# Optimization experiments

Measured on AMD Instinct MI355X. Metric: run time of the kernel, lower is better.

Reference implementation:

```python
import jax, jax.numpy as jnp
import numpy as np

B, D, L, H = 8192, 1024, 64, 256

def setup_inputs() -> dict:
    key = jax.random.key(0)
    k_x, k_w1, k_b1, k_w2, k_b2 = jax.random.split(key, 5)
    # Stacked per-label parameters (equivalent to L independent 2-layer MLPs)
    lim1 = 1.0 / np.sqrt(D)
    lim2 = 1.0 / np.sqrt(H)
    return {
        "x": jax.random.normal(k_x, (B, D), dtype=jnp.float32),
        "W1": jax.random.uniform(k_w1, (L, D, H), dtype=jnp.float32, minval=-lim1, maxval=lim1),
        "b1": jax.random.uniform(k_b1, (L, H), dtype=jnp.float32, minval=-lim1, maxval=lim1),
        "W2": jax.random.uniform(k_w2, (L, H), dtype=jnp.float32, minval=-lim2, maxval=lim2),
        "b2": jax.random.uniform(k_b2, (L,), dtype=jnp.float32, minval=-lim2, maxval=lim2),
    }

def reference(x, W1, b1, W2, b2):
    # h: [B, L, H] = relu(x @ W1_l + b1_l) for every label l, as one batched GEMM
    h = jax.nn.relu(jnp.einsum('bd,ldh->blh', x, W1) + b1[None, :, :])
    # out: [B, L] = h_l @ W2_l + b2_l  (second Linear has output dim 1, squeezed)
    out = jnp.einsum('blh,lh->bl', h, W2) + b2[None, :]
    return out
```

## Files before the change

kernel.cpp:

```cpp
#include <hip/hip_runtime.h>
#include <stdint.h>

#define B_SZ 8192
#define D_SZ 1024
#define L_SZ 64
#define H_SZ 256

#define BM 256
#define BN 256
#define BK 64
#define NT (D_SZ / BK)

typedef __attribute__((ext_vector_type(8))) __bf16 bf16x8;
typedef __attribute__((ext_vector_type(4))) float f32x4;

typedef __attribute__((address_space(1))) void as1_void;
typedef __attribute__((address_space(3))) void as3_void;

static __device__ __forceinline__ void gload_lds16(const void* g, void* l) {
    __builtin_amdgcn_global_load_lds((as1_void*)g, (as3_void*)l, 16, 0, 0);
}

static __device__ __forceinline__ unsigned short f2bf(float f) {
    uint32_t u = __builtin_bit_cast(uint32_t, f);
    u += 0x7fffu + ((u >> 16) & 1u);
    return (unsigned short)(u >> 16);
}

__global__ void cvt_x_kernel(const float* __restrict__ x, unsigned short* __restrict__ xb) {
    int i = blockIdx.x * blockDim.x + threadIdx.x;
    const float4 v = reinterpret_cast<const float4*>(x)[i];
    ushort4 o;
    o.x = f2bf(v.x); o.y = f2bf(v.y); o.z = f2bf(v.z); o.w = f2bf(v.w);
    reinterpret_cast<ushort4*>(xb)[i] = o;
}

__global__ void transpose_w1_kernel(const float* __restrict__ w1, unsigned short* __restrict__ w1t) {
    __shared__ float tile[64][65];
    int b = blockIdx.x;
    int l  = b >> 6;
    int dt = (b >> 2) & 15;
    int ht = b & 3;
    int tx = threadIdx.x & 63;
    int ty = threadIdx.x >> 6;
    const float* src = w1 + (size_t)l * (D_SZ * H_SZ);
    #pragma unroll
    for (int r = 0; r < 64; r += 4)
        tile[r + ty][tx] = src[(size_t)(dt * 64 + r + ty) * H_SZ + ht * 64 + tx];
    __syncthreads();
    unsigned short* dst = w1t + (size_t)l * (H_SZ * D_SZ);
    #pragma unroll
    for (int r = 0; r < 64; r += 4)
        dst[(size_t)(ht * 64 + r + ty) * D_SZ + dt * 64 + tx] = f2bf(tile[tx][r + ty]);
}


#define SBAR asm volatile("s_barrier" ::: "memory")
#define VMW(n) asm volatile("s_waitcnt vmcnt(" #n ")" ::: "memory")

#define DS_READ_A(c, quad) do { \
    _Pragma("unroll") for (int j = 0; j < 2; ++j) { \
        const int rowh = ((quad)*2 + j)*16 + rl; \
        _Pragma("unroll") for (int ks = 0; ks < 2; ++ks) { \
            const int slot = (ks*4 + g) ^ (rowh & 7); \
            af[ks][j] = *reinterpret_cast<const bf16x8*>( \
                reinterpret_cast<const char*>(&ldsAB[c][0][wr][0]) + rowh*128 + slot*16); \
        } } } while(0)

#define DS_READ_B(c) do { \
    _Pragma("unroll") for (int nf = 0; nf < 4; ++nf) { \
        const int rowb = wc*64 + nf*16 + rl; \
        const int bh = rowb >> 7; \
        const int rowh = rowb & 127; \
        _Pragma("unroll") for (int ks = 0; ks < 2; ++ks) { \
            const int slot = (ks*4 + g) ^ (rowh & 7); \
            bf[ks][nf] = *reinterpret_cast<const bf16x8*>( \
                reinterpret_cast<const char*>(&ldsAB[c][1][bh][0]) + rowh*128 + slot*16); \
        } } } while(0)

#define MFMA_QUAD(quad) do { \
    __builtin_amdgcn_s_setprio(1); \
    _Pragma("unroll") for (int ks = 0; ks < 2; ++ks) \
    _Pragma("unroll") for (int j = 0; j < 2; ++j) \
    _Pragma("unroll") for (int nf = 0; nf < 4; ++nf) \
        acc[(quad)*2 + j][nf] = __builtin_amdgcn_mfma_f32_16x16x32_bf16( \
            af[ks][j], bf[ks][nf], acc[(quad)*2 + j][nf], 0, 0, 0); \
    __builtin_amdgcn_s_setprio(0); } while(0)

#define STAGE_A(t, h) do { \
    gload_lds16(aSrc[h][0] + (size_t)(t)*BK, &ldsAB[(t)&1][0][h][(wid*64)*8]); \
    gload_lds16(aSrc[h][1] + (size_t)(t)*BK, &ldsAB[(t)&1][0][h][(512 + wid*64)*8]); } while(0)

#define STAGE_B(t, h) do { \
    gload_lds16(bSrc[h][0] + (size_t)(t)*BK, &ldsAB[(t)&1][1][h][(wid*64)*8]); \
    gload_lds16(bSrc[h][1] + (size_t)(t)*BK, &ldsAB[(t)&1][1][h][(512 + wid*64)*8]); } while(0)

__global__ __launch_bounds__(512, 2) void ffn_gemm_kernel(
    const unsigned short* __restrict__ xb,
    const unsigned short* __restrict__ w1t,
    const float* __restrict__ b1,
    const float* __restrict__ w2,
    const float* __restrict__ b2,
    float* __restrict__ out)
{
    __shared__ unsigned short ldsAB[2][2][2][128 * 64];

    const int bid = blockIdx.x;
    const int wg  = ((bid & 7) << 8) + (bid >> 3);
    const int l   = wg >> 5;
    const int m0  = (wg & 31) * BM;

    const int tid  = threadIdx.x;
    const int wid  = tid >> 6;
    const int lane = tid & 63;
    const int wr   = wid >> 2;
    const int wc   = wid & 3;
    const int g    = lane >> 4;
    const int rl   = lane & 15;

    const unsigned short* aSrc[2][2];
    const unsigned short* bSrc[2][2];
    #pragma unroll
    for (int h = 0; h < 2; ++h)
        #pragma unroll
        for (int c2 = 0; c2 < 2; ++c2) {
            const int q  = c2 * 512 + tid;
            const int r  = q >> 3;
            const int kg = (q & 7) ^ (r & 7);
            aSrc[h][c2] = xb  + (size_t)(m0 + h * 128 + r) * D_SZ + kg * 8;
            bSrc[h][c2] = w1t + ((size_t)l * H_SZ + h * 128 + r) * D_SZ + kg * 8;
        }

    f32x4 acc[8][4];
    #pragma unroll
    for (int m = 0; m < 8; ++m)
        #pragma unroll
        for (int n = 0; n < 4; ++n) {
            acc[m][n][0] = 0.f; acc[m][n][1] = 0.f;
            acc[m][n][2] = 0.f; acc[m][n][3] = 0.f;
        }

    bf16x8 af[2][2], bf[2][4];

    STAGE_B(0, 0); STAGE_B(0, 1);
    STAGE_A(0, 0); STAGE_A(0, 1);
    STAGE_B(1, 0); STAGE_B(1, 1);
    VMW(4);
    SBAR;

    #pragma unroll 1
    for (int i = 0; i < 7; ++i) {
        const int t1 = 2 * i + 1, t2 = 2 * i + 2, t3 = 2 * i + 3;
        DS_READ_B(0); DS_READ_A(0, 0); STAGE_A(t1, 0); SBAR; MFMA_QUAD(0); SBAR;
        DS_READ_A(0, 1); STAGE_A(t1, 1); SBAR; MFMA_QUAD(1); SBAR;
        DS_READ_A(0, 2); STAGE_B(t2, 0); SBAR; MFMA_QUAD(2); SBAR;
        DS_READ_A(0, 3); STAGE_B(t2, 1); SBAR; MFMA_QUAD(3); VMW(4); SBAR;
        DS_READ_B(1); DS_READ_A(1, 0); STAGE_A(t2, 0); SBAR; MFMA_QUAD(0); SBAR;
        DS_READ_A(1, 1); STAGE_A(t2, 1); SBAR; MFMA_QUAD(1); SBAR;
        DS_READ_A(1, 2); STAGE_B(t3, 0); SBAR; MFMA_QUAD(2); SBAR;
        DS_READ_A(1, 3); STAGE_B(t3, 1); SBAR; MFMA_QUAD(3); VMW(4); SBAR;
    }
    DS_READ_B(0); DS_READ_A(0, 0); STAGE_A(15, 0); SBAR; MFMA_QUAD(0); SBAR;
    DS_READ_A(0, 1); STAGE_A(15, 1); SBAR; MFMA_QUAD(1); SBAR;
    DS_READ_A(0, 2); SBAR; MFMA_QUAD(2); SBAR;
    DS_READ_A(0, 3); SBAR; MFMA_QUAD(3); VMW(0); SBAR;
    DS_READ_B(1); DS_READ_A(1, 0); SBAR; MFMA_QUAD(0); SBAR;
    DS_READ_A(1, 1); SBAR; MFMA_QUAD(1); SBAR;
    DS_READ_A(1, 2); SBAR; MFMA_QUAD(2); SBAR;
    DS_READ_A(1, 3); SBAR; MFMA_QUAD(3); SBAR;

    float b1v[4], w2v[4];
    #pragma unroll
    for (int nf = 0; nf < 4; ++nf) {
        const int col = wc * 64 + nf * 16 + rl;
        b1v[nf] = b1[l * H_SZ + col];
        w2v[nf] = w2[l * H_SZ + col];
    }
    __syncthreads();
    float* partLds = (float*)&ldsAB[0][0][0][0];
    #pragma unroll
    for (int mf = 0; mf < 8; ++mf) {
        #pragma unroll
        for (int r = 0; r < 4; ++r) {
            float p = 0.f;
            #pragma unroll
            for (int nf = 0; nf < 4; ++nf) {
                float v = acc[mf][nf][r] + b1v[nf];
                v = fmaxf(v, 0.f);
                p += v * w2v[nf];
            }
            p += __shfl_xor(p, 1);
            p += __shfl_xor(p, 2);
            p += __shfl_xor(p, 4);
            p += __shfl_xor(p, 8);
            if (rl == 0)
                partLds[((wr * 128) + mf * 16 + g * 4 + r) * 4 + wc] = p;
        }
    }
    __syncthreads();
    if (tid < BM) {
        float s = b2[l];
        #pragma unroll
        for (int w = 0; w < 4; ++w) s += partLds[tid * 4 + w];
        out[(size_t)(m0 + tid) * L_SZ + l] = s;
    }
}

extern "C" void kernel_launch(void* const* d_in, const int* in_sizes, int n_in,
                              void* d_out, int out_size, void* d_ws, size_t ws_size,
                              hipStream_t stream) {
    const float* x  = (const float*)d_in[0];
    const float* W1 = (const float*)d_in[1];
    const float* b1 = (const float*)d_in[2];
    const float* W2 = (const float*)d_in[3];
    const float* b2 = (const float*)d_in[4];
    float* out = (float*)d_out;

    unsigned short* xb  = (unsigned short*)d_ws;
    unsigned short* w1t = xb + (size_t)B_SZ * D_SZ;

    cvt_x_kernel<<<(B_SZ * D_SZ / 4) / 256, 256, 0, stream>>>(x, xb);
    transpose_w1_kernel<<<L_SZ * 16 * 4, 256, 0, stream>>>(W1, w1t);
    ffn_gemm_kernel<<<(B_SZ / BM) * L_SZ, 512, 0, stream>>>(xb, w1t, b1, W2, b2, out);
}
```

Baseline: 294.3 us.

## Make GEMM persistent over eight M-tiles, prefetching next tile during tail

The launch drops from 2048 workgroups to 256. Each workgroup now loops over eight consecutive 256-row M tiles for a fixed label and keeps bias/W2 values in registers. The last k-steps of one tile issue the loads for the next tile's first k-tiles, which hides the pipeline prologue and epilogue. The trade-off is only 256 workgroups on the GPU (about one per CU), so the occupancy of two blocks per CU is lost, plus a larger serial epilogue per workgroup. The final iteration prefetches past the tile range, into rows of the next group or past the end of xb.

```diff
diff --git a/kernel.cpp b/kernel.cpp
--- a/kernel.cpp
+++ b/kernel.cpp
@@ -9,7 +9,6 @@
 #define BM 256
 #define BN 256
 #define BK 64
-#define NT (D_SZ / BK)
 
 typedef __attribute__((ext_vector_type(8))) __bf16 bf16x8;
 typedef __attribute__((ext_vector_type(4))) float f32x4;
@@ -91,6 +90,10 @@
     gload_lds16(aSrc[h][0] + (size_t)(t)*BK, &ldsAB[(t)&1][0][h][(wid*64)*8]); \
     gload_lds16(aSrc[h][1] + (size_t)(t)*BK, &ldsAB[(t)&1][0][h][(512 + wid*64)*8]); } while(0)
 
+#define STAGE_AN(h) do { \
+    gload_lds16(aSrc[h][0] + ADV, &ldsAB[0][0][h][(wid*64)*8]); \
+    gload_lds16(aSrc[h][1] + ADV, &ldsAB[0][0][h][(512 + wid*64)*8]); } while(0)
+
 #define STAGE_B(t, h) do { \
     gload_lds16(bSrc[h][0] + (size_t)(t)*BK, &ldsAB[(t)&1][1][h][(wid*64)*8]); \
     gload_lds16(bSrc[h][1] + (size_t)(t)*BK, &ldsAB[(t)&1][1][h][(512 + wid*64)*8]); } while(0)
@@ -104,11 +107,12 @@
     float* __restrict__ out)
 {
     __shared__ unsigned short ldsAB[2][2][2][128 * 64];
+    __shared__ float partLds[256][4];
 
     const int bid = blockIdx.x;
-    const int wg  = ((bid & 7) << 8) + (bid >> 3);
-    const int l   = wg >> 5;
-    const int m0  = (wg & 31) * BM;
+    const int l   = (bid & 7) * 8 + ((bid >> 3) & 7);
+    const int gi  = bid >> 6;
+    const int m00 = gi * 8 * BM;
 
     const int tid  = threadIdx.x;
     const int wid  = tid >> 6;
@@ -118,6 +122,8 @@
     const int g    = lane >> 4;
     const int rl   = lane & 15;
 
+    const size_t ADV = (size_t)BM * D_SZ;
+
     const unsigned short* aSrc[2][2];
     const unsigned short* bSrc[2][2];
     #pragma unroll
@@ -127,19 +133,20 @@
             const int q  = c2 * 512 + tid;
             const int r  = q >> 3;
             const int kg = (q & 7) ^ (r & 7);
-            aSrc[h][c2] = xb  + (size_t)(m0 + h * 128 + r) * D_SZ + kg * 8;
+            aSrc[h][c2] = xb  + (size_t)(m00 + h * 128 + r) * D_SZ + kg * 8;
             bSrc[h][c2] = w1t + ((size_t)l * H_SZ + h * 128 + r) * D_SZ + kg * 8;
         }
 
+    float b1v[4], w2v[4];
+    #pragma unroll
+    for (int nf = 0; nf < 4; ++nf) {
+        const int col = wc * 64 + nf * 16 + rl;
+        b1v[nf] = b1[l * H_SZ + col];
+        w2v[nf] = w2[l * H_SZ + col];
+    }
+    const float b2v = b2[l];
+
     f32x4 acc[8][4];
-    #pragma unroll
-    for (int m = 0; m < 8; ++m)
-        #pragma unroll
-        for (int n = 0; n < 4; ++n) {
-            acc[m][n][0] = 0.f; acc[m][n][1] = 0.f;
-            acc[m][n][2] = 0.f; acc[m][n][3] = 0.f;
-        }
-
     bf16x8 af[2][2], bf[2][4];
 
     STAGE_B(0, 0); STAGE_B(0, 1);
@@ -149,61 +156,72 @@
     SBAR;
 
     #pragma unroll 1
-    for (int i = 0; i < 7; ++i) {
-        const int t1 = 2 * i + 1, t2 = 2 * i + 2, t3 = 2 * i + 3;
-        DS_READ_B(0); DS_READ_A(0, 0); STAGE_A(t1, 0); SBAR; MFMA_QUAD(0); SBAR;
-        DS_READ_A(0, 1); STAGE_A(t1, 1); SBAR; MFMA_QUAD(1); SBAR;
-        DS_READ_A(0, 2); STAGE_B(t2, 0); SBAR; MFMA_QUAD(2); SBAR;
-        DS_READ_A(0, 3); STAGE_B(t2, 1); SBAR; MFMA_QUAD(3); VMW(4); SBAR;
-        DS_READ_B(1); DS_READ_A(1, 0); STAGE_A(t2, 0); SBAR; MFMA_QUAD(0); SBAR;
-        DS_READ_A(1, 1); STAGE_A(t2, 1); SBAR; MFMA_QUAD(1); SBAR;
-        DS_READ_A(1, 2); STAGE_B(t3, 0); SBAR; MFMA_QUAD(2); SBAR;
-        DS_READ_A(1, 3); STAGE_B(t3, 1); SBAR; MFMA_QUAD(3); VMW(4); SBAR;
+    for (int o = 0; o < 8; ++o) {
+        #pragma unroll
+        for (int m = 0; m < 8; ++m)
+            #pragma unroll
+            for (int n = 0; n < 4; ++n) {
+                acc[m][n][0] = 0.f; acc[m][n][1] = 0.f;
+                acc[m][n][2] = 0.f; acc[m][n][3] = 0.f;
+            }
+
+        #pragma unroll 1
+        for (int i = 0; i < 7; ++i) {
+            const int t1 = 2 * i + 1, t2 = 2 * i + 2, t3 = 2 * i + 3;
+            DS_READ_B(0); DS_READ_A(0, 0); STAGE_A(t1, 0); SBAR; MFMA_QUAD(0); SBAR;
+            DS_READ_A(0, 1); STAGE_A(t1, 1); SBAR; MFMA_QUAD(1); SBAR;
+            DS_READ_A(0, 2); STAGE_B(t2, 0); SBAR; MFMA_QUAD(2); SBAR;
+            DS_READ_A(0, 3); STAGE_B(t2, 1); SBAR; MFMA_QUAD(3); VMW(4); SBAR;
+            DS_READ_B(1); DS_READ_A(1, 0); STAGE_A(t2, 0); SBAR; MFMA_QUAD(0); SBAR;
+            DS_READ_A(1, 1); STAGE_A(t2, 1); SBAR; MFMA_QUAD(1); SBAR;
+            DS_READ_A(1, 2); STAGE_B(t3, 0); SBAR; MFMA_QUAD(2); SBAR;
+            DS_READ_A(1, 3); STAGE_B(t3, 1); SBAR; MFMA_QUAD(3); VMW(4); SBAR;
+        }
+        DS_READ_B(0); DS_READ_A(0, 0); STAGE_A(15, 0); SBAR; MFMA_QUAD(0); SBAR;
+        DS_READ_A(0, 1); STAGE_A(15, 1); SBAR; MFMA_QUAD(1); SBAR;
+        DS_READ_A(0, 2); STAGE_B(0, 0); SBAR; MFMA_QUAD(2); SBAR;
+        DS_READ_A(0, 3); STAGE_B(0, 1); SBAR; MFMA_QUAD(3); VMW(4); SBAR;
+        DS_READ_B(1); DS_READ_A(1, 0); STAGE_AN(0); SBAR; MFMA_QUAD(0); SBAR;
+        DS_READ_A(1, 1); STAGE_AN(1); SBAR; MFMA_QUAD(1); SBAR;
+        DS_READ_A(1, 2); STAGE_B(1, 0); SBAR; MFMA_QUAD(2); SBAR;
+        DS_READ_A(1, 3); STAGE_B(1, 1); SBAR; MFMA_QUAD(3); VMW(4); SBAR;
+
+        const int m0 = m00 + o * BM;
+        #pragma unroll
+        for (int mf = 0; mf < 8; ++mf) {
+            #pragma unroll
+            for (int r = 0; r < 4; ++r) {
+                float p = 0.f;
+                #pragma unroll
+                for (int nf = 0; nf < 4; ++nf) {
+                    float v = acc[mf][nf][r] + b1v[nf];
+                    v = fmaxf(v, 0.f);
+                    p += v * w2v[nf];
+                }
+                p += __shfl_xor(p, 1);
+                p += __shfl_xor(p, 2);
+                p += __shfl_xor(p, 4);
+                p += __shfl_xor(p, 8);
+                if (rl == 0)
+                    partLds[wr * 128 + mf * 16 + g * 4 + r][wc] = p;
+            }
+        }
+        __syncthreads();
+        if (tid < BM) {
+            float s = b2v;
+            #pragma unroll
+            for (int w = 0; w < 4; ++w) s += partLds[tid][w];
+            out[(size_t)(m0 + tid) * L_SZ + l] = s;
+        }
+        __syncthreads();
+
+        #pragma unroll
+        for (int h = 0; h < 2; ++h)
+            #pragma unroll
+            for (int c2 = 0; c2 < 2; ++c2)
+                aSrc[h][c2] += ADV;
     }
-    DS_READ_B(0); DS_READ_A(0, 0); STAGE_A(15, 0); SBAR; MFMA_QUAD(0); SBAR;
-    DS_READ_A(0, 1); STAGE_A(15, 1); SBAR; MFMA_QUAD(1); SBAR;
-    DS_READ_A(0, 2); SBAR; MFMA_QUAD(2); SBAR;
-    DS_READ_A(0, 3); SBAR; MFMA_QUAD(3); VMW(0); SBAR;
-    DS_READ_B(1); DS_READ_A(1, 0); SBAR; MFMA_QUAD(0); SBAR;
-    DS_READ_A(1, 1); SBAR; MFMA_QUAD(1); SBAR;
-    DS_READ_A(1, 2); SBAR; MFMA_QUAD(2); SBAR;
-    DS_READ_A(1, 3); SBAR; MFMA_QUAD(3); SBAR;
-
-    float b1v[4], w2v[4];
-    #pragma unroll
-    for (int nf = 0; nf < 4; ++nf) {
-        const int col = wc * 64 + nf * 16 + rl;
-        b1v[nf] = b1[l * H_SZ + col];
-        w2v[nf] = w2[l * H_SZ + col];
-    }
-    __syncthreads();
-    float* partLds = (float*)&ldsAB[0][0][0][0];
-    #pragma unroll
-    for (int mf = 0; mf < 8; ++mf) {
-        #pragma unroll
-        for (int r = 0; r < 4; ++r) {
-            float p = 0.f;
-            #pragma unroll
-            for (int nf = 0; nf < 4; ++nf) {
-                float v = acc[mf][nf][r] + b1v[nf];
-                v = fmaxf(v, 0.f);
-                p += v * w2v[nf];
-            }
-            p += __shfl_xor(p, 1);
-            p += __shfl_xor(p, 2);
-            p += __shfl_xor(p, 4);
-            p += __shfl_xor(p, 8);
-            if (rl == 0)
-                partLds[((wr * 128) + mf * 16 + g * 4 + r) * 4 + wc] = p;
-        }
-    }
-    __syncthreads();
-    if (tid < BM) {
-        float s = b2[l];
-        #pragma unroll
-        for (int w = 0; w < 4; ++w) s += partLds[tid * 4 + w];
-        out[(size_t)(m0 + tid) * L_SZ + l] = s;
-    }
+    VMW(0);
 }
 
 extern "C" void kernel_launch(void* const* d_in, const int* in_sizes, int n_in,
@@ -221,5 +239,5 @@
 
     cvt_x_kernel<<<(B_SZ * D_SZ / 4) / 256, 256, 0, stream>>>(x, xb);
     transpose_w1_kernel<<<L_SZ * 16 * 4, 256, 0, stream>>>(W1, w1t);
-    ffn_gemm_kernel<<<(B_SZ / BM) * L_SZ, 512, 0, stream>>>(xb, w1t, b1, W2, b2, out);
-}
+    ffn_gemm_kernel<<<256, 512, 0, stream>>>(xb, w1t, b1, W2, b2, out);
+}
```

Result: slower. 305.6 us (+3.8%).

## Load W1 tiles directly into registers instead of staging through LDS

Applied to the files above, without the earlier changes.

The B operand (transposed W1) is no longer staged through shared memory. Each thread loads its MFMA B fragments straight from global memory into two alternating register buffers, one per K-step parity, which halves LDS use and removes the B ds_reads. The cost is that the global B loads are uncoalesced 16-byte gathers per lane, duplicated across the two wave rows. It also adds register pressure under the 2-blocks-per-CU launch bound and changes the vmcnt accounting. Bias and W2 loads are hoisted before the main loop.

```diff
diff --git a/kernel.cpp b/kernel.cpp
--- a/kernel.cpp
+++ b/kernel.cpp
@@ -9,7 +9,6 @@
 #define BM 256
 #define BN 256
 #define BK 64
-#define NT (D_SZ / BK)
 
 typedef __attribute__((ext_vector_type(8))) __bf16 bf16x8;
 typedef __attribute__((ext_vector_type(4))) float f32x4;
@@ -64,36 +63,27 @@
         _Pragma("unroll") for (int ks = 0; ks < 2; ++ks) { \
             const int slot = (ks*4 + g) ^ (rowh & 7); \
             af[ks][j] = *reinterpret_cast<const bf16x8*>( \
-                reinterpret_cast<const char*>(&ldsAB[c][0][wr][0]) + rowh*128 + slot*16); \
+                reinterpret_cast<const char*>(&ldsA[c][wr][0]) + rowh*128 + slot*16); \
         } } } while(0)
 
-#define DS_READ_B(c) do { \
-    _Pragma("unroll") for (int nf = 0; nf < 4; ++nf) { \
-        const int rowb = wc*64 + nf*16 + rl; \
-        const int bh = rowb >> 7; \
-        const int rowh = rowb & 127; \
-        _Pragma("unroll") for (int ks = 0; ks < 2; ++ks) { \
-            const int slot = (ks*4 + g) ^ (rowh & 7); \
-            bf[ks][nf] = *reinterpret_cast<const bf16x8*>( \
-                reinterpret_cast<const char*>(&ldsAB[c][1][bh][0]) + rowh*128 + slot*16); \
-        } } } while(0)
-
-#define MFMA_QUAD(quad) do { \
+#define LOAD_B(breg, t) do { \
+    _Pragma("unroll") for (int nf = 0; nf < 4; ++nf) \
+    _Pragma("unroll") for (int ks = 0; ks < 2; ++ks) \
+        breg[ks][nf] = bPtr[nf][(size_t)(t) * 8 + ks * 4]; \
+} while(0)
+
+#define MFMA_QUAD(quad, breg) do { \
     __builtin_amdgcn_s_setprio(1); \
     _Pragma("unroll") for (int ks = 0; ks < 2; ++ks) \
     _Pragma("unroll") for (int j = 0; j < 2; ++j) \
     _Pragma("unroll") for (int nf = 0; nf < 4; ++nf) \
         acc[(quad)*2 + j][nf] = __builtin_amdgcn_mfma_f32_16x16x32_bf16( \
-            af[ks][j], bf[ks][nf], acc[(quad)*2 + j][nf], 0, 0, 0); \
+            af[ks][j], breg[ks][nf], acc[(quad)*2 + j][nf], 0, 0, 0); \
     __builtin_amdgcn_s_setprio(0); } while(0)
 
 #define STAGE_A(t, h) do { \
-    gload_lds16(aSrc[h][0] + (size_t)(t)*BK, &ldsAB[(t)&1][0][h][(wid*64)*8]); \
-    gload_lds16(aSrc[h][1] + (size_t)(t)*BK, &ldsAB[(t)&1][0][h][(512 + wid*64)*8]); } while(0)
-
-#define STAGE_B(t, h) do { \
-    gload_lds16(bSrc[h][0] + (size_t)(t)*BK, &ldsAB[(t)&1][1][h][(wid*64)*8]); \
-    gload_lds16(bSrc[h][1] + (size_t)(t)*BK, &ldsAB[(t)&1][1][h][(512 + wid*64)*8]); } while(0)
+    gload_lds16(aSrc[h][0] + (size_t)(t)*BK, &ldsA[(t)&1][h][(wid*64)*8]); \
+    gload_lds16(aSrc[h][1] + (size_t)(t)*BK, &ldsA[(t)&1][h][(512 + wid*64)*8]); } while(0)
 
 __global__ __launch_bounds__(512, 2) void ffn_gemm_kernel(
     const unsigned short* __restrict__ xb,
@@ -103,7 +93,8 @@
     const float* __restrict__ b2,
     float* __restrict__ out)
 {
-    __shared__ unsigned short ldsAB[2][2][2][128 * 64];
+    __shared__ unsigned short ldsA[2][2][128 * 64];
+    __shared__ float partRed[256][4];
 
     const int bid = blockIdx.x;
     const int wg  = ((bid & 7) << 8) + (bid >> 3);
@@ -119,7 +110,6 @@
     const int rl   = lane & 15;
 
     const unsigned short* aSrc[2][2];
-    const unsigned short* bSrc[2][2];
     #pragma unroll
     for (int h = 0; h < 2; ++h)
         #pragma unroll
@@ -127,9 +117,25 @@
             const int q  = c2 * 512 + tid;
             const int r  = q >> 3;
             const int kg = (q & 7) ^ (r & 7);
-            aSrc[h][c2] = xb  + (size_t)(m0 + h * 128 + r) * D_SZ + kg * 8;
-            bSrc[h][c2] = w1t + ((size_t)l * H_SZ + h * 128 + r) * D_SZ + kg * 8;
+            aSrc[h][c2] = xb + (size_t)(m0 + h * 128 + r) * D_SZ + kg * 8;
         }
+
+    const bf16x8* bPtr[4];
+    #pragma unroll
+    for (int nf = 0; nf < 4; ++nf) {
+        const int col = wc * 64 + nf * 16 + rl;
+        bPtr[nf] = reinterpret_cast<const bf16x8*>(
+                       w1t + ((size_t)l * H_SZ + col) * D_SZ) + g;
+    }
+
+    float b1v[4], w2v[4];
+    #pragma unroll
+    for (int nf = 0; nf < 4; ++nf) {
+        const int col = wc * 64 + nf * 16 + rl;
+        b1v[nf] = b1[l * H_SZ + col];
+        w2v[nf] = w2[l * H_SZ + col];
+    }
+    const float b2v = b2[l];
 
     f32x4 acc[8][4];
     #pragma unroll
@@ -140,44 +146,38 @@
             acc[m][n][2] = 0.f; acc[m][n][3] = 0.f;
         }
 
-    bf16x8 af[2][2], bf[2][4];
-
-    STAGE_B(0, 0); STAGE_B(0, 1);
+    bf16x8 af[2][2];
+    bf16x8 bregE[2][4], bregO[2][4];
+
     STAGE_A(0, 0); STAGE_A(0, 1);
-    STAGE_B(1, 0); STAGE_B(1, 1);
-    VMW(4);
+    LOAD_B(bregE, 0);
+    LOAD_B(bregO, 1);
+    VMW(8);
     SBAR;
 
     #pragma unroll 1
     for (int i = 0; i < 7; ++i) {
-        const int t1 = 2 * i + 1, t2 = 2 * i + 2, t3 = 2 * i + 3;
-        DS_READ_B(0); DS_READ_A(0, 0); STAGE_A(t1, 0); SBAR; MFMA_QUAD(0); SBAR;
-        DS_READ_A(0, 1); STAGE_A(t1, 1); SBAR; MFMA_QUAD(1); SBAR;
-        DS_READ_A(0, 2); STAGE_B(t2, 0); SBAR; MFMA_QUAD(2); SBAR;
-        DS_READ_A(0, 3); STAGE_B(t2, 1); SBAR; MFMA_QUAD(3); VMW(4); SBAR;
-        DS_READ_B(1); DS_READ_A(1, 0); STAGE_A(t2, 0); SBAR; MFMA_QUAD(0); SBAR;
-        DS_READ_A(1, 1); STAGE_A(t2, 1); SBAR; MFMA_QUAD(1); SBAR;
-        DS_READ_A(1, 2); STAGE_B(t3, 0); SBAR; MFMA_QUAD(2); SBAR;
-        DS_READ_A(1, 3); STAGE_B(t3, 1); SBAR; MFMA_QUAD(3); VMW(4); SBAR;
-    }
-    DS_READ_B(0); DS_READ_A(0, 0); STAGE_A(15, 0); SBAR; MFMA_QUAD(0); SBAR;
-    DS_READ_A(0, 1); STAGE_A(15, 1); SBAR; MFMA_QUAD(1); SBAR;
-    DS_READ_A(0, 2); SBAR; MFMA_QUAD(2); SBAR;
-    DS_READ_A(0, 3); SBAR; MFMA_QUAD(3); VMW(0); SBAR;
-    DS_READ_B(1); DS_READ_A(1, 0); SBAR; MFMA_QUAD(0); SBAR;
-    DS_READ_A(1, 1); SBAR; MFMA_QUAD(1); SBAR;
-    DS_READ_A(1, 2); SBAR; MFMA_QUAD(2); SBAR;
-    DS_READ_A(1, 3); SBAR; MFMA_QUAD(3); SBAR;
-
-    float b1v[4], w2v[4];
-    #pragma unroll
-    for (int nf = 0; nf < 4; ++nf) {
-        const int col = wc * 64 + nf * 16 + rl;
-        b1v[nf] = b1[l * H_SZ + col];
-        w2v[nf] = w2[l * H_SZ + col];
-    }
-    __syncthreads();
-    float* partLds = (float*)&ldsAB[0][0][0][0];
+        const int e = 2 * i, o = 2 * i + 1;
+        DS_READ_A(0, 0); STAGE_A(e + 1, 0); SBAR; MFMA_QUAD(0, bregE); SBAR;
+        DS_READ_A(0, 1); STAGE_A(e + 1, 1); SBAR; MFMA_QUAD(1, bregE); SBAR;
+        DS_READ_A(0, 2);                    SBAR; MFMA_QUAD(2, bregE); SBAR;
+        DS_READ_A(0, 3);                    SBAR; MFMA_QUAD(3, bregE);
+        LOAD_B(bregE, e + 2); VMW(8); SBAR;
+        DS_READ_A(1, 0); STAGE_A(o + 1, 0); SBAR; MFMA_QUAD(0, bregO); SBAR;
+        DS_READ_A(1, 1); STAGE_A(o + 1, 1); SBAR; MFMA_QUAD(1, bregO); SBAR;
+        DS_READ_A(1, 2);                    SBAR; MFMA_QUAD(2, bregO); SBAR;
+        DS_READ_A(1, 3);                    SBAR; MFMA_QUAD(3, bregO);
+        LOAD_B(bregO, o + 2); VMW(8); SBAR;
+    }
+    DS_READ_A(0, 0); STAGE_A(15, 0); SBAR; MFMA_QUAD(0, bregE); SBAR;
+    DS_READ_A(0, 1); STAGE_A(15, 1); SBAR; MFMA_QUAD(1, bregE); SBAR;
+    DS_READ_A(0, 2);                 SBAR; MFMA_QUAD(2, bregE); SBAR;
+    DS_READ_A(0, 3);                 SBAR; MFMA_QUAD(3, bregE); VMW(0); SBAR;
+    DS_READ_A(1, 0);                 SBAR; MFMA_QUAD(0, bregO); SBAR;
+    DS_READ_A(1, 1);                 SBAR; MFMA_QUAD(1, bregO); SBAR;
+    DS_READ_A(1, 2);                 SBAR; MFMA_QUAD(2, bregO); SBAR;
+    DS_READ_A(1, 3);                 SBAR; MFMA_QUAD(3, bregO);
+
     #pragma unroll
     for (int mf = 0; mf < 8; ++mf) {
         #pragma unroll
@@ -194,14 +194,14 @@
             p += __shfl_xor(p, 4);
             p += __shfl_xor(p, 8);
             if (rl == 0)
-                partLds[((wr * 128) + mf * 16 + g * 4 + r) * 4 + wc] = p;
+                partRed[wr * 128 + mf * 16 + g * 4 + r][wc] = p;
         }
     }
     __syncthreads();
     if (tid < BM) {
-        float s = b2[l];
-        #pragma unroll
-        for (int w = 0; w < 4; ++w) s += partLds[tid * 4 + w];
+        float s = b2v;
+        #pragma unroll
+        for (int w = 0; w < 4; ++w) s += partRed[tid][w];
         out[(size_t)(m0 + tid) * L_SZ + l] = s;
     }
 }
```

Result: slower. 442.3 us (+50.3%).

## Double-buffer B fragments in registers and interleave their LDS reads with MFMA quads

Applied to the files above, without the earlier changes.

B-operand fragments are split into even and odd register sets, and their LDS reads are spread across the MFMA quads of the previous buffer instead of being issued in one burst at the start of each half-iteration. Epilogue bias and weight loads are hoisted before the main loop, and a dedicated LDS reduction buffer replaces reuse of the A/B staging buffers, so the final syncthreads before the reduction is dropped. The intent is to hide LDS read latency behind MFMA work. The cost is more VGPRs for the second B set, extra LDS for the reduction buffer, and changed vmcnt waits, which could hurt occupancy at 2 blocks per CU.

```diff
diff --git a/kernel.cpp b/kernel.cpp
--- a/kernel.cpp
+++ b/kernel.cpp
@@ -9,7 +9,6 @@
 #define BM 256
 #define BN 256
 #define BK 64
-#define NT (D_SZ / BK)
 
 typedef __attribute__((ext_vector_type(8))) __bf16 bf16x8;
 typedef __attribute__((ext_vector_type(4))) float f32x4;
@@ -64,36 +63,37 @@
         _Pragma("unroll") for (int ks = 0; ks < 2; ++ks) { \
             const int slot = (ks*4 + g) ^ (rowh & 7); \
             af[ks][j] = *reinterpret_cast<const bf16x8*>( \
-                reinterpret_cast<const char*>(&ldsAB[c][0][wr][0]) + rowh*128 + slot*16); \
+                reinterpret_cast<const char*>(&ldsA[c][wr][0]) + rowh*128 + slot*16); \
         } } } while(0)
 
-#define DS_READ_B(c) do { \
-    _Pragma("unroll") for (int nf = 0; nf < 4; ++nf) { \
+#define BN2(c, dst, jj) do { \
+    const int ks = (jj) >> 1; \
+    _Pragma("unroll") for (int p = 0; p < 2; ++p) { \
+        const int nf = ((jj) & 1) * 2 + p; \
         const int rowb = wc*64 + nf*16 + rl; \
         const int bh = rowb >> 7; \
         const int rowh = rowb & 127; \
-        _Pragma("unroll") for (int ks = 0; ks < 2; ++ks) { \
-            const int slot = (ks*4 + g) ^ (rowh & 7); \
-            bf[ks][nf] = *reinterpret_cast<const bf16x8*>( \
-                reinterpret_cast<const char*>(&ldsAB[c][1][bh][0]) + rowh*128 + slot*16); \
-        } } } while(0)
-
-#define MFMA_QUAD(quad) do { \
+        const int slot = (ks*4 + g) ^ (rowh & 7); \
+        dst[ks][nf] = *reinterpret_cast<const bf16x8*>( \
+            reinterpret_cast<const char*>(&ldsB[c][bh][0]) + rowh*128 + slot*16); \
+    } } while(0)
+
+#define MFMA_QUAD(quad, bfX) do { \
     __builtin_amdgcn_s_setprio(1); \
     _Pragma("unroll") for (int ks = 0; ks < 2; ++ks) \
     _Pragma("unroll") for (int j = 0; j < 2; ++j) \
     _Pragma("unroll") for (int nf = 0; nf < 4; ++nf) \
         acc[(quad)*2 + j][nf] = __builtin_amdgcn_mfma_f32_16x16x32_bf16( \
-            af[ks][j], bf[ks][nf], acc[(quad)*2 + j][nf], 0, 0, 0); \
+            af[ks][j], bfX[ks][nf], acc[(quad)*2 + j][nf], 0, 0, 0); \
     __builtin_amdgcn_s_setprio(0); } while(0)
 
 #define STAGE_A(t, h) do { \
-    gload_lds16(aSrc[h][0] + (size_t)(t)*BK, &ldsAB[(t)&1][0][h][(wid*64)*8]); \
-    gload_lds16(aSrc[h][1] + (size_t)(t)*BK, &ldsAB[(t)&1][0][h][(512 + wid*64)*8]); } while(0)
+    gload_lds16(aSrc[h][0] + (size_t)(t)*BK, &ldsA[(t)&1][h][(wid*64)*8]); \
+    gload_lds16(aSrc[h][1] + (size_t)(t)*BK, &ldsA[(t)&1][h][(512 + wid*64)*8]); } while(0)
 
 #define STAGE_B(t, h) do { \
-    gload_lds16(bSrc[h][0] + (size_t)(t)*BK, &ldsAB[(t)&1][1][h][(wid*64)*8]); \
-    gload_lds16(bSrc[h][1] + (size_t)(t)*BK, &ldsAB[(t)&1][1][h][(512 + wid*64)*8]); } while(0)
+    gload_lds16(bSrc[h][0] + (size_t)(t)*BK, &ldsB[(t)&1][h][(wid*64)*8]); \
+    gload_lds16(bSrc[h][1] + (size_t)(t)*BK, &ldsB[(t)&1][h][(512 + wid*64)*8]); } while(0)
 
 __global__ __launch_bounds__(512, 2) void ffn_gemm_kernel(
     const unsigned short* __restrict__ xb,
@@ -103,7 +103,9 @@
     const float* __restrict__ b2,
     float* __restrict__ out)
 {
-    __shared__ unsigned short ldsAB[2][2][2][128 * 64];
+    __shared__ unsigned short ldsA[2][2][128 * 64];
+    __shared__ unsigned short ldsB[2][2][128 * 64];
+    __shared__ float partRed[256][4];
 
     const int bid = blockIdx.x;
     const int wg  = ((bid & 7) << 8) + (bid >> 3);
@@ -131,6 +133,15 @@
             bSrc[h][c2] = w1t + ((size_t)l * H_SZ + h * 128 + r) * D_SZ + kg * 8;
         }
 
+    float b1v[4], w2v[4];
+    #pragma unroll
+    for (int nf = 0; nf < 4; ++nf) {
+        const int col = wc * 64 + nf * 16 + rl;
+        b1v[nf] = b1[l * H_SZ + col];
+        w2v[nf] = w2[l * H_SZ + col];
+    }
+    const float b2v = b2[l];
+
     f32x4 acc[8][4];
     #pragma unroll
     for (int m = 0; m < 8; ++m)
@@ -140,44 +151,38 @@
             acc[m][n][2] = 0.f; acc[m][n][3] = 0.f;
         }
 
-    bf16x8 af[2][2], bf[2][4];
+    bf16x8 af[2][2];
+    bf16x8 bfE[2][4], bfO[2][4];
 
     STAGE_B(0, 0); STAGE_B(0, 1);
     STAGE_A(0, 0); STAGE_A(0, 1);
     STAGE_B(1, 0); STAGE_B(1, 1);
-    VMW(4);
+    VMW(0);
     SBAR;
+    BN2(0, bfE, 0); BN2(0, bfE, 1); BN2(0, bfE, 2); BN2(0, bfE, 3);
 
     #pragma unroll 1
     for (int i = 0; i < 7; ++i) {
         const int t1 = 2 * i + 1, t2 = 2 * i + 2, t3 = 2 * i + 3;
-        DS_READ_B(0); DS_READ_A(0, 0); STAGE_A(t1, 0); SBAR; MFMA_QUAD(0); SBAR;
-        DS_READ_A(0, 1); STAGE_A(t1, 1); SBAR; MFMA_QUAD(1); SBAR;
-        DS_READ_A(0, 2); STAGE_B(t2, 0); SBAR; MFMA_QUAD(2); SBAR;
-        DS_READ_A(0, 3); STAGE_B(t2, 1); SBAR; MFMA_QUAD(3); VMW(4); SBAR;
-        DS_READ_B(1); DS_READ_A(1, 0); STAGE_A(t2, 0); SBAR; MFMA_QUAD(0); SBAR;
-        DS_READ_A(1, 1); STAGE_A(t2, 1); SBAR; MFMA_QUAD(1); SBAR;
-        DS_READ_A(1, 2); STAGE_B(t3, 0); SBAR; MFMA_QUAD(2); SBAR;
-        DS_READ_A(1, 3); STAGE_B(t3, 1); SBAR; MFMA_QUAD(3); VMW(4); SBAR;
-    }
-    DS_READ_B(0); DS_READ_A(0, 0); STAGE_A(15, 0); SBAR; MFMA_QUAD(0); SBAR;
-    DS_READ_A(0, 1); STAGE_A(15, 1); SBAR; MFMA_QUAD(1); SBAR;
-    DS_READ_A(0, 2); SBAR; MFMA_QUAD(2); SBAR;
-    DS_READ_A(0, 3); SBAR; MFMA_QUAD(3); VMW(0); SBAR;
-    DS_READ_B(1); DS_READ_A(1, 0); SBAR; MFMA_QUAD(0); SBAR;
-    DS_READ_A(1, 1); SBAR; MFMA_QUAD(1); SBAR;
-    DS_READ_A(1, 2); SBAR; MFMA_QUAD(2); SBAR;
-    DS_READ_A(1, 3); SBAR; MFMA_QUAD(3); SBAR;
-
-    float b1v[4], w2v[4];
-    #pragma unroll
-    for (int nf = 0; nf < 4; ++nf) {
-        const int col = wc * 64 + nf * 16 + rl;
-        b1v[nf] = b1[l * H_SZ + col];
-        w2v[nf] = w2[l * H_SZ + col];
-    }
-    __syncthreads();
-    float* partLds = (float*)&ldsAB[0][0][0][0];
+        DS_READ_A(0, 0); BN2(1, bfO, 0); STAGE_A(t1, 0); SBAR; MFMA_QUAD(0, bfE); SBAR;
+        DS_READ_A(0, 1); BN2(1, bfO, 1); STAGE_A(t1, 1); SBAR; MFMA_QUAD(1, bfE); SBAR;
+        DS_READ_A(0, 2); BN2(1, bfO, 2); STAGE_B(t2, 0); SBAR; MFMA_QUAD(2, bfE); SBAR;
+        DS_READ_A(0, 3); BN2(1, bfO, 3); STAGE_B(t2, 1); SBAR; MFMA_QUAD(3, bfE); VMW(4); SBAR;
+        DS_READ_A(1, 0);                                 STAGE_A(t2, 0); SBAR; MFMA_QUAD(0, bfO); VMW(2); SBAR;
+        DS_READ_A(1, 1); BN2(0, bfE, 0);                 STAGE_A(t2, 1); SBAR; MFMA_QUAD(1, bfO); SBAR;
+        DS_READ_A(1, 2); BN2(0, bfE, 1); BN2(0, bfE, 2); STAGE_B(t3, 0); SBAR; MFMA_QUAD(2, bfO); SBAR;
+        DS_READ_A(1, 3); BN2(0, bfE, 3);                 STAGE_B(t3, 1); SBAR; MFMA_QUAD(3, bfO); VMW(4); SBAR;
+    }
+    VMW(0);
+    DS_READ_A(0, 0);                                 STAGE_A(15, 0); SBAR; MFMA_QUAD(0, bfE); SBAR;
+    DS_READ_A(0, 1); BN2(1, bfO, 0); BN2(1, bfO, 1); STAGE_A(15, 1); SBAR; MFMA_QUAD(1, bfE); SBAR;
+    DS_READ_A(0, 2); BN2(1, bfO, 2); BN2(1, bfO, 3);                 SBAR; MFMA_QUAD(2, bfE); SBAR;
+    DS_READ_A(0, 3);                                                 SBAR; MFMA_QUAD(3, bfE); VMW(0); SBAR;
+    DS_READ_A(1, 0); SBAR; MFMA_QUAD(0, bfO); SBAR;
+    DS_READ_A(1, 1); SBAR; MFMA_QUAD(1, bfO); SBAR;
+    DS_READ_A(1, 2); SBAR; MFMA_QUAD(2, bfO); SBAR;
+    DS_READ_A(1, 3); SBAR; MFMA_QUAD(3, bfO);
+
     #pragma unroll
     for (int mf = 0; mf < 8; ++mf) {
         #pragma unroll
@@ -194,14 +199,14 @@
             p += __shfl_xor(p, 4);
             p += __shfl_xor(p, 8);
             if (rl == 0)
-                partLds[((wr * 128) + mf * 16 + g * 4 + r) * 4 + wc] = p;
+                partRed[wr * 128 + mf * 16 + g * 4 + r][wc] = p;
         }
     }
     __syncthreads();
     if (tid < BM) {
-        float s = b2[l];
-        #pragma unroll
-        for (int w = 0; w < 4; ++w) s += partLds[tid * 4 + w];
+        float s = b2v;
+        #pragma unroll
+        for (int w = 0; w < 4; ++w) s += partRed[tid][w];
         out[(size_t)(m0 + tid) * L_SZ + l] = s;
     }
 }
```

After: 376.8 us. 28.0% more time.
